# Optimization experiments

Measured on AMD Instinct MI355X. Metric: run time of the kernel, lower is better.

The kernel has to match this reference:

```python
import jax, jax.numpy as jnp
import numpy as np

M = 150        # AR2 tail-fit window
LAM = 1e-3     # ridge regularizer in the 2x2 solve
CLIP_K = 4.0   # soft clip multiplier
H = 96         # forecast horizon (base_model.H)


def setup_inputs() -> dict:
    key = jax.random.key(0)
    k1, k2 = jax.random.split(key)
    x = jax.random.normal(k1, (32, 512, 2048), dtype=jnp.float32)
    W = jax.random.normal(k2, (2048, 96), dtype=jnp.float32) * 0.02
    return {"x": x, "W": W}


def _ar2_forecast(x):
    # x: (B, C, L); closed-form AR2 fit on last M samples, vectorized over (B, C)
    y = x[..., -M:]                     # (B, C, M)
    Y = y[..., 2:]                      # targets
    p1 = y[..., 1:-1]
    p2 = y[..., :-2]
    s = lambda a, b: jnp.sum(a * b, axis=-1)
    A11 = s(p1, p1) + LAM
    A22 = s(p2, p2) + LAM
    A12 = s(p1, p2)
    b1 = s(p1, Y)
    b2 = s(p2, Y)
    det = A11 * A22 - A12 * A12
    a1 = (b1 * A22 - b2 * A12) / det    # (B, C)
    a2 = (A11 * b2 - A12 * b1) / det

    def step(carry, _):
        y1, y2 = carry
        yn = a1 * y1 + a2 * y2
        return (yn, y1), yn

    _, out = jax.lax.scan(step, (x[..., -1], x[..., -2]), None, length=H)
    return jnp.moveaxis(out, 0, -1)     # (B, C, H)


def reference(x, W):
    # AR2 part is computed on detached history in the original (numpy round-trip)
    Yb = jax.lax.stop_gradient(_ar2_forecast(x))
    d_hat = jnp.einsum('bcl,lh->bch', x, W)          # base model: per-channel linear head
    y_hat = Yb + d_hat
    last = x[..., -1:]                               # (B, C, 1), broadcasts over H
    hstd = jnp.maximum(jnp.std(x, axis=-1, ddof=1, keepdims=True), 1e-6)  # torch unbiased std
    return jnp.clip(y_hat, last - CLIP_K * hstd, last + CLIP_K * hstd)
```

## Files before the change

### kernel.cpp

```cpp
#include <hip/hip_runtime.h>
#include <math.h>

constexpr int L     = 2048;
constexpr int NH    = 96;
constexpr int MLEN  = 150;
constexpr int NAR   = 148;
constexpr float LAM    = 0.001f;
constexpr float CLIP_K = 4.0f;

constexpr int TM     = 16;
constexpr int KM     = 64;
constexpr int MSTEPS = L / KM;

typedef __attribute__((ext_vector_type(8))) short short8;
typedef __attribute__((ext_vector_type(4))) float floatx4;

__device__ inline short f2bf(float f) {
    union { float f; unsigned u; } v; v.f = f;
    unsigned r = v.u + 0x7FFFu + ((v.u >> 16) & 1u);
    return (short)(r >> 16);
}

__global__ __launch_bounds__(256) void wt_kernel(
    const float* __restrict__ W, short* __restrict__ Wt)
{
    int idx = blockIdx.x * 256 + threadIdx.x;
    int n = idx >> 11;
    int k = idx & 2047;
    Wt[idx] = f2bf(W[k * NH + n]);
}

__global__ __launch_bounds__(256, 4) void gemm_ar2_kernel(
    const float* __restrict__ x, const short* __restrict__ Wt,
    float* __restrict__ out)
{
    __shared__ float As[2][TM * KM];
    __shared__ short Bs[2][NH * KM];
    __shared__ float Ys[TM][NH + 1];
    __shared__ float los[TM], his[TM];
    __shared__ float s2[TM], q2[TM];

    const int t    = threadIdx.x;
    const int lane = t & 63;
    const int wv   = t >> 6;
    const int g    = wv & 1;
    const int e    = wv >> 1;
    const int m    = lane & 15;
    const int quad = lane >> 4;
    const int row0 = blockIdx.x * TM;

    const int rA = t >> 4, chA = t & 15;
    const float* pa = x + (size_t)(row0 + rA) * L
                        + ((chA >> 3) * 32 + ((chA & 7) ^ (rA & 7)) * 4);

    const int cB0 = wv * 192 + lane, cB1 = cB0 + 64, cB2 = cB0 + 128;
    const short* pb0 = Wt + (size_t)(cB0 >> 3) * L + (((cB0 & 7) ^ ((cB0 >> 3) & 7)) * 8);
    const short* pb1 = Wt + (size_t)(cB1 >> 3) * L + (((cB1 & 7) ^ ((cB1 >> 3) & 7)) * 8);
    const short* pb2 = Wt + (size_t)(cB2 >> 3) * L + (((cB2 & 7) ^ ((cB2 >> 3) & 7)) * 8);

    floatx4 acc[3];
    #pragma unroll
    for (int jj = 0; jj < 3; ++jj) acc[jj] = floatx4{0.f, 0.f, 0.f, 0.f};
    float sum = 0.f, sumsq = 0.f;

    const int pA0 = (2 * quad)     ^ (m & 7);
    const int pA1 = (2 * quad + 1) ^ (m & 7);

    auto stage = [&](int buf, int k0) {
        __builtin_amdgcn_global_load_lds(
            (const __attribute__((address_space(1))) unsigned int*)(pa + k0),
            (__attribute__((address_space(3))) unsigned int*)&As[buf][wv * 256], 16, 0, 0);
        __builtin_amdgcn_global_load_lds(
            (const __attribute__((address_space(1))) unsigned int*)(pb0 + k0),
            (__attribute__((address_space(3))) unsigned int*)&Bs[buf][wv * 1536], 16, 0, 0);
        __builtin_amdgcn_global_load_lds(
            (const __attribute__((address_space(1))) unsigned int*)(pb1 + k0),
            (__attribute__((address_space(3))) unsigned int*)&Bs[buf][wv * 1536 + 512], 16, 0, 0);
        __builtin_amdgcn_global_load_lds(
            (const __attribute__((address_space(1))) unsigned int*)(pb2 + k0),
            (__attribute__((address_space(3))) unsigned int*)&Bs[buf][wv * 1536 + 1024], 16, 0, 0);
    };

    stage(0, 0);

    for (int s = 0; s < MSTEPS; ++s) {
        const int cur = s & 1;
        __syncthreads();
        if (s + 1 < MSTEPS) stage(cur ^ 1, (s + 1) * KM);

        float4 f0 = *(const float4*)&As[cur][m * KM + e * 32 + pA0 * 4];
        float4 f1 = *(const float4*)&As[cur][m * KM + e * 32 + pA1 * 4];

        if (g == 0) {
            sum  += ((f0.x + f0.y) + (f0.z + f0.w))
                  + ((f1.x + f1.y) + (f1.z + f1.w));
            sumsq = fmaf(f0.x, f0.x, sumsq); sumsq = fmaf(f0.y, f0.y, sumsq);
            sumsq = fmaf(f0.z, f0.z, sumsq); sumsq = fmaf(f0.w, f0.w, sumsq);
            sumsq = fmaf(f1.x, f1.x, sumsq); sumsq = fmaf(f1.y, f1.y, sumsq);
            sumsq = fmaf(f1.z, f1.z, sumsq); sumsq = fmaf(f1.w, f1.w, sumsq);
        }

        short8 af;
        af[0] = f2bf(f0.x); af[1] = f2bf(f0.y); af[2] = f2bf(f0.z); af[3] = f2bf(f0.w);
        af[4] = f2bf(f1.x); af[5] = f2bf(f1.y); af[6] = f2bf(f1.z); af[7] = f2bf(f1.w);

        const int bch = ((e * 4 + quad) ^ (m & 7)) * 8;
        #pragma unroll
        for (int jj = 0; jj < 3; ++jj) {
            short8 bf = *(const short8*)&Bs[cur][(g * 48 + jj * 16 + m) * KM + bch];
            acc[jj] = __builtin_amdgcn_mfma_f32_16x16x32_bf16(af, bf, acc[jj], 0, 0, 0);
        }
    }

    float* ar = (float*)&Bs[0][0];
    if (e == 1) {
        #pragma unroll
        for (int jj = 0; jj < 3; ++jj)
            #pragma unroll
            for (int reg = 0; reg < 4; ++reg)
                ar[(g * 64 + lane) * 12 + jj * 4 + reg] = acc[jj][reg];
        if (g == 0) {
            float su = sum, sq = sumsq;
            su += __shfl_xor(su, 16); su += __shfl_xor(su, 32);
            sq += __shfl_xor(sq, 16); sq += __shfl_xor(sq, 32);
            if (quad == 0) { s2[m] = su; q2[m] = sq; }
        }
    }
    __syncthreads();

    if (e == 0) {
        #pragma unroll
        for (int jj = 0; jj < 3; ++jj)
            #pragma unroll
            for (int reg = 0; reg < 4; ++reg)
                acc[jj][reg] += ar[(g * 64 + lane) * 12 + jj * 4 + reg];

        if (g == 0) {
            sum   += __shfl_xor(sum,   16); sum   += __shfl_xor(sum,   32);
            sumsq += __shfl_xor(sumsq, 16); sumsq += __shfl_xor(sumsq, 32);

            const float* ytail = x + (size_t)(row0 + m) * L + (L - MLEN);
            float A11 = 0.f, A22 = 0.f, A12 = 0.f, b1 = 0.f, b2 = 0.f;
            for (int i = quad; i < NAR; i += 4) {
                float p2v = ytail[i];
                float p1v = ytail[i + 1];
                float Yv  = ytail[i + 2];
                A11 = fmaf(p1v, p1v, A11);
                A22 = fmaf(p2v, p2v, A22);
                A12 = fmaf(p1v, p2v, A12);
                b1  = fmaf(p1v, Yv,  b1);
                b2  = fmaf(p2v, Yv,  b2);
            }
            A11 += __shfl_xor(A11, 16); A11 += __shfl_xor(A11, 32);
            A22 += __shfl_xor(A22, 16); A22 += __shfl_xor(A22, 32);
            A12 += __shfl_xor(A12, 16); A12 += __shfl_xor(A12, 32);
            b1  += __shfl_xor(b1,  16); b1  += __shfl_xor(b1,  32);
            b2  += __shfl_xor(b2,  16); b2  += __shfl_xor(b2,  32);

            if (quad == 0) {
                sum   += s2[m];
                sumsq += q2[m];
                A11 += LAM; A22 += LAM;
                float det = A11 * A22 - A12 * A12;
                float a1c = (b1 * A22 - b2 * A12) / det;
                float a2c = (A11 * b2 - A12 * b1) / det;

                float last = ytail[MLEN - 1];
                float y1 = last;
                float y2 = ytail[MLEN - 2];
                for (int n = 0; n < NH; ++n) {
                    float yn = a1c * y1 + a2c * y2;
                    Ys[m][n] = yn;
                    y2 = y1; y1 = yn;
                }
                float var  = (sumsq - sum * sum * (1.0f / L)) * (1.0f / (L - 1));
                float hstd = fmaxf(sqrtf(fmaxf(var, 0.f)), 1e-6f);
                los[m] = last - CLIP_K * hstd;
                his[m] = last + CLIP_K * hstd;
            }
        }
    }
    __syncthreads();

    if (e == 0) {
        #pragma unroll
        for (int reg = 0; reg < 4; ++reg) {
            int rl = quad * 4 + reg;
            float lo = los[rl], hi = his[rl];
            #pragma unroll
            for (int jj = 0; jj < 3; ++jj) {
                int c = (3 * g + jj) * 16 + m;
                float v = acc[jj][reg] + Ys[rl][c];
                v = fminf(fmaxf(v, lo), hi);
                out[(size_t)(row0 + rl) * NH + c] = v;
            }
        }
    }
}

extern "C" void kernel_launch(void* const* d_in, const int* in_sizes, int n_in,
                              void* d_out, int out_size, void* d_ws, size_t ws_size,
                              hipStream_t stream) {
    const float* x = (const float*)d_in[0];
    const float* W = (const float*)d_in[1];
    float* out = (float*)d_out;
    short* Wt  = (short*)d_ws;

    wt_kernel<<<dim3((NH * L) / 256), dim3(256), 0, stream>>>(W, Wt);

    const int rows = 32 * 512;
    gemm_ar2_kernel<<<dim3(rows / TM), dim3(256), 0, stream>>>(x, Wt, out);
}
```

Measured before the change: 209.9 us.

## Replace LDS-staged GEMM with register-prefetched direct loads and split-K across waves

Each block previously staged x and bf16 W tiles into LDS with async global-to-LDS loads, double-buffered, with a block barrier every K step. Now every wave owns a contiguous quarter of K (512 elements) and computes all 96 output columns. It loads its A and B fragments straight from global memory into registers, prefetching the next step, so the per-step barriers and LDS traffic are gone. Partial accumulators and the row sums are reduced through LDS once at the end. Wave 0 alone runs the AR2 fit and the clipped store, which also drops a barrier. The trade-off is higher register use (6 accumulators plus prefetched fragments) and narrower, strided global loads that rely on cache hits for W.

```diff
diff --git a/kernel.cpp b/kernel.cpp
--- a/kernel.cpp
+++ b/kernel.cpp
@@ -8,9 +8,10 @@
 constexpr float LAM    = 0.001f;
 constexpr float CLIP_K = 4.0f;
 
-constexpr int TM     = 16;
-constexpr int KM     = 64;
-constexpr int MSTEPS = L / KM;
+constexpr int TM    = 16;
+constexpr int KQ    = 512;
+constexpr int KSTEP = 32;
+constexpr int NSTEP = KQ / KSTEP;
 
 typedef __attribute__((ext_vector_type(8))) short short8;
 typedef __attribute__((ext_vector_type(4))) float floatx4;
@@ -34,162 +35,136 @@
     const float* __restrict__ x, const short* __restrict__ Wt,
     float* __restrict__ out)
 {
-    __shared__ float As[2][TM * KM];
-    __shared__ short Bs[2][NH * KM];
+    __shared__ float ar[3][6][64][4];
+    __shared__ float s2[3][TM], q2[3][TM];
     __shared__ float Ys[TM][NH + 1];
     __shared__ float los[TM], his[TM];
-    __shared__ float s2[TM], q2[TM];
 
     const int t    = threadIdx.x;
     const int lane = t & 63;
-    const int wv   = t >> 6;
-    const int g    = wv & 1;
-    const int e    = wv >> 1;
+    const int e    = t >> 6;
     const int m    = lane & 15;
     const int quad = lane >> 4;
     const int row0 = blockIdx.x * TM;
 
-    const int rA = t >> 4, chA = t & 15;
-    const float* pa = x + (size_t)(row0 + rA) * L
-                        + ((chA >> 3) * 32 + ((chA & 7) ^ (rA & 7)) * 4);
+    const float* pa = x + (size_t)(row0 + m) * L + e * KQ + quad * 8;
+    const short* pb[6];
+    #pragma unroll
+    for (int jj = 0; jj < 6; ++jj)
+        pb[jj] = Wt + (size_t)(jj * 16 + m) * L + e * KQ + quad * 8;
 
-    const int cB0 = wv * 192 + lane, cB1 = cB0 + 64, cB2 = cB0 + 128;
-    const short* pb0 = Wt + (size_t)(cB0 >> 3) * L + (((cB0 & 7) ^ ((cB0 >> 3) & 7)) * 8);
-    const short* pb1 = Wt + (size_t)(cB1 >> 3) * L + (((cB1 & 7) ^ ((cB1 >> 3) & 7)) * 8);
-    const short* pb2 = Wt + (size_t)(cB2 >> 3) * L + (((cB2 & 7) ^ ((cB2 >> 3) & 7)) * 8);
-
-    floatx4 acc[3];
+    floatx4 acc[6];
     #pragma unroll
-    for (int jj = 0; jj < 3; ++jj) acc[jj] = floatx4{0.f, 0.f, 0.f, 0.f};
+    for (int jj = 0; jj < 6; ++jj) acc[jj] = floatx4{0.f, 0.f, 0.f, 0.f};
     float sum = 0.f, sumsq = 0.f;
 
-    const int pA0 = (2 * quad)     ^ (m & 7);
-    const int pA1 = (2 * quad + 1) ^ (m & 7);
+    float4 ca0 = *(const float4*)(pa);
+    float4 ca1 = *(const float4*)(pa + 4);
+    short8 cb[6];
+    #pragma unroll
+    for (int jj = 0; jj < 6; ++jj) cb[jj] = *(const short8*)(pb[jj]);
 
-    auto stage = [&](int buf, int k0) {
-        __builtin_amdgcn_global_load_lds(
-            (const __attribute__((address_space(1))) unsigned int*)(pa + k0),
-            (__attribute__((address_space(3))) unsigned int*)&As[buf][wv * 256], 16, 0, 0);
-        __builtin_amdgcn_global_load_lds(
-            (const __attribute__((address_space(1))) unsigned int*)(pb0 + k0),
-            (__attribute__((address_space(3))) unsigned int*)&Bs[buf][wv * 1536], 16, 0, 0);
-        __builtin_amdgcn_global_load_lds(
-            (const __attribute__((address_space(1))) unsigned int*)(pb1 + k0),
-            (__attribute__((address_space(3))) unsigned int*)&Bs[buf][wv * 1536 + 512], 16, 0, 0);
-        __builtin_amdgcn_global_load_lds(
-            (const __attribute__((address_space(1))) unsigned int*)(pb2 + k0),
-            (__attribute__((address_space(3))) unsigned int*)&Bs[buf][wv * 1536 + 1024], 16, 0, 0);
-    };
+    #pragma unroll 4
+    for (int s = 0; s < NSTEP; ++s) {
+        const int off = (s + 1 < NSTEP ? s + 1 : s) * KSTEP;
+        float4 na0 = *(const float4*)(pa + off);
+        float4 na1 = *(const float4*)(pa + off + 4);
+        short8 nb[6];
+        #pragma unroll
+        for (int jj = 0; jj < 6; ++jj) nb[jj] = *(const short8*)(pb[jj] + off);
 
-    stage(0, 0);
-
-    for (int s = 0; s < MSTEPS; ++s) {
-        const int cur = s & 1;
-        __syncthreads();
-        if (s + 1 < MSTEPS) stage(cur ^ 1, (s + 1) * KM);
-
-        float4 f0 = *(const float4*)&As[cur][m * KM + e * 32 + pA0 * 4];
-        float4 f1 = *(const float4*)&As[cur][m * KM + e * 32 + pA1 * 4];
-
-        if (g == 0) {
-            sum  += ((f0.x + f0.y) + (f0.z + f0.w))
-                  + ((f1.x + f1.y) + (f1.z + f1.w));
-            sumsq = fmaf(f0.x, f0.x, sumsq); sumsq = fmaf(f0.y, f0.y, sumsq);
-            sumsq = fmaf(f0.z, f0.z, sumsq); sumsq = fmaf(f0.w, f0.w, sumsq);
-            sumsq = fmaf(f1.x, f1.x, sumsq); sumsq = fmaf(f1.y, f1.y, sumsq);
-            sumsq = fmaf(f1.z, f1.z, sumsq); sumsq = fmaf(f1.w, f1.w, sumsq);
-        }
+        sum  += ((ca0.x + ca0.y) + (ca0.z + ca0.w))
+              + ((ca1.x + ca1.y) + (ca1.z + ca1.w));
+        sumsq = fmaf(ca0.x, ca0.x, sumsq); sumsq = fmaf(ca0.y, ca0.y, sumsq);
+        sumsq = fmaf(ca0.z, ca0.z, sumsq); sumsq = fmaf(ca0.w, ca0.w, sumsq);
+        sumsq = fmaf(ca1.x, ca1.x, sumsq); sumsq = fmaf(ca1.y, ca1.y, sumsq);
+        sumsq = fmaf(ca1.z, ca1.z, sumsq); sumsq = fmaf(ca1.w, ca1.w, sumsq);
 
         short8 af;
-        af[0] = f2bf(f0.x); af[1] = f2bf(f0.y); af[2] = f2bf(f0.z); af[3] = f2bf(f0.w);
-        af[4] = f2bf(f1.x); af[5] = f2bf(f1.y); af[6] = f2bf(f1.z); af[7] = f2bf(f1.w);
+        af[0] = f2bf(ca0.x); af[1] = f2bf(ca0.y); af[2] = f2bf(ca0.z); af[3] = f2bf(ca0.w);
+        af[4] = f2bf(ca1.x); af[5] = f2bf(ca1.y); af[6] = f2bf(ca1.z); af[7] = f2bf(ca1.w);
 
-        const int bch = ((e * 4 + quad) ^ (m & 7)) * 8;
         #pragma unroll
-        for (int jj = 0; jj < 3; ++jj) {
-            short8 bf = *(const short8*)&Bs[cur][(g * 48 + jj * 16 + m) * KM + bch];
-            acc[jj] = __builtin_amdgcn_mfma_f32_16x16x32_bf16(af, bf, acc[jj], 0, 0, 0);
-        }
+        for (int jj = 0; jj < 6; ++jj)
+            acc[jj] = __builtin_amdgcn_mfma_f32_16x16x32_bf16(af, cb[jj], acc[jj], 0, 0, 0);
+
+        ca0 = na0; ca1 = na1;
+        #pragma unroll
+        for (int jj = 0; jj < 6; ++jj) cb[jj] = nb[jj];
     }
 
-    float* ar = (float*)&Bs[0][0];
-    if (e == 1) {
+    if (e > 0) {
         #pragma unroll
-        for (int jj = 0; jj < 3; ++jj)
+        for (int jj = 0; jj < 6; ++jj)
             #pragma unroll
             for (int reg = 0; reg < 4; ++reg)
-                ar[(g * 64 + lane) * 12 + jj * 4 + reg] = acc[jj][reg];
-        if (g == 0) {
-            float su = sum, sq = sumsq;
-            su += __shfl_xor(su, 16); su += __shfl_xor(su, 32);
-            sq += __shfl_xor(sq, 16); sq += __shfl_xor(sq, 32);
-            if (quad == 0) { s2[m] = su; q2[m] = sq; }
-        }
+                ar[e - 1][jj][lane][reg] = acc[jj][reg];
+        float su = sum, sq = sumsq;
+        su += __shfl_xor(su, 16); su += __shfl_xor(su, 32);
+        sq += __shfl_xor(sq, 16); sq += __shfl_xor(sq, 32);
+        if (quad == 0) { s2[e - 1][m] = su; q2[e - 1][m] = sq; }
     }
     __syncthreads();
 
     if (e == 0) {
         #pragma unroll
-        for (int jj = 0; jj < 3; ++jj)
+        for (int q = 0; q < 3; ++q)
             #pragma unroll
-            for (int reg = 0; reg < 4; ++reg)
-                acc[jj][reg] += ar[(g * 64 + lane) * 12 + jj * 4 + reg];
+            for (int jj = 0; jj < 6; ++jj)
+                #pragma unroll
+                for (int reg = 0; reg < 4; ++reg)
+                    acc[jj][reg] += ar[q][jj][lane][reg];
 
-        if (g == 0) {
-            sum   += __shfl_xor(sum,   16); sum   += __shfl_xor(sum,   32);
-            sumsq += __shfl_xor(sumsq, 16); sumsq += __shfl_xor(sumsq, 32);
+        sum   += __shfl_xor(sum,   16); sum   += __shfl_xor(sum,   32);
+        sumsq += __shfl_xor(sumsq, 16); sumsq += __shfl_xor(sumsq, 32);
 
-            const float* ytail = x + (size_t)(row0 + m) * L + (L - MLEN);
-            float A11 = 0.f, A22 = 0.f, A12 = 0.f, b1 = 0.f, b2 = 0.f;
-            for (int i = quad; i < NAR; i += 4) {
-                float p2v = ytail[i];
-                float p1v = ytail[i + 1];
-                float Yv  = ytail[i + 2];
-                A11 = fmaf(p1v, p1v, A11);
-                A22 = fmaf(p2v, p2v, A22);
-                A12 = fmaf(p1v, p2v, A12);
-                b1  = fmaf(p1v, Yv,  b1);
-                b2  = fmaf(p2v, Yv,  b2);
+        const float* ytail = x + (size_t)(row0 + m) * L + (L - MLEN);
+        float A11 = 0.f, A22 = 0.f, A12 = 0.f, b1 = 0.f, b2 = 0.f;
+        for (int i = quad; i < NAR; i += 4) {
+            float p2v = ytail[i];
+            float p1v = ytail[i + 1];
+            float Yv  = ytail[i + 2];
+            A11 = fmaf(p1v, p1v, A11);
+            A22 = fmaf(p2v, p2v, A22);
+            A12 = fmaf(p1v, p2v, A12);
+            b1  = fmaf(p1v, Yv,  b1);
+            b2  = fmaf(p2v, Yv,  b2);
+        }
+        A11 += __shfl_xor(A11, 16); A11 += __shfl_xor(A11, 32);
+        A22 += __shfl_xor(A22, 16); A22 += __shfl_xor(A22, 32);
+        A12 += __shfl_xor(A12, 16); A12 += __shfl_xor(A12, 32);
+        b1  += __shfl_xor(b1,  16); b1  += __shfl_xor(b1,  32);
+        b2  += __shfl_xor(b2,  16); b2  += __shfl_xor(b2,  32);
+
+        if (quad == 0) {
+            sum   += s2[0][m] + s2[1][m] + s2[2][m];
+            sumsq += q2[0][m] + q2[1][m] + q2[2][m];
+            A11 += LAM; A22 += LAM;
+            float det = A11 * A22 - A12 * A12;
+            float a1c = (b1 * A22 - b2 * A12) / det;
+            float a2c = (A11 * b2 - A12 * b1) / det;
+
+            float last = ytail[MLEN - 1];
+            float y1 = last;
+            float y2 = ytail[MLEN - 2];
+            for (int n = 0; n < NH; ++n) {
+                float yn = a1c * y1 + a2c * y2;
+                Ys[m][n] = yn;
+                y2 = y1; y1 = yn;
             }
-            A11 += __shfl_xor(A11, 16); A11 += __shfl_xor(A11, 32);
-            A22 += __shfl_xor(A22, 16); A22 += __shfl_xor(A22, 32);
-            A12 += __shfl_xor(A12, 16); A12 += __shfl_xor(A12, 32);
-            b1  += __shfl_xor(b1,  16); b1  += __shfl_xor(b1,  32);
-            b2  += __shfl_xor(b2,  16); b2  += __shfl_xor(b2,  32);
+            float var  = (sumsq - sum * sum * (1.0f / L)) * (1.0f / (L - 1));
+            float hstd = fmaxf(sqrtf(fmaxf(var, 0.f)), 1e-6f);
+            los[m] = last - CLIP_K * hstd;
+            his[m] = last + CLIP_K * hstd;
+        }
 
-            if (quad == 0) {
-                sum   += s2[m];
-                sumsq += q2[m];
-                A11 += LAM; A22 += LAM;
-                float det = A11 * A22 - A12 * A12;
-                float a1c = (b1 * A22 - b2 * A12) / det;
-                float a2c = (A11 * b2 - A12 * b1) / det;
-
-                float last = ytail[MLEN - 1];
-                float y1 = last;
-                float y2 = ytail[MLEN - 2];
-                for (int n = 0; n < NH; ++n) {
-                    float yn = a1c * y1 + a2c * y2;
-                    Ys[m][n] = yn;
-                    y2 = y1; y1 = yn;
-                }
-                float var  = (sumsq - sum * sum * (1.0f / L)) * (1.0f / (L - 1));
-                float hstd = fmaxf(sqrtf(fmaxf(var, 0.f)), 1e-6f);
-                los[m] = last - CLIP_K * hstd;
-                his[m] = last + CLIP_K * hstd;
-            }
-        }
-    }
-    __syncthreads();
-
-    if (e == 0) {
         #pragma unroll
         for (int reg = 0; reg < 4; ++reg) {
             int rl = quad * 4 + reg;
             float lo = los[rl], hi = his[rl];
             #pragma unroll
-            for (int jj = 0; jj < 3; ++jj) {
-                int c = (3 * g + jj) * 16 + m;
+            for (int jj = 0; jj < 6; ++jj) {
+                int c = jj * 16 + m;
                 float v = acc[jj][reg] + Ys[rl][c];
                 v = fminf(fmaxf(v, lo), hi);
                 out[(size_t)(row0 + rl) * NH + c] = v;
```

After: 233.1 us. 11.0% more time.
